# Kernel optimization log

Measured on AMD Instinct MI355X. Metric: run time of the kernel, lower is better.

Reference implementation:

```python
import jax, jax.numpy as jnp
import numpy as np

D = 1024
N_HEAD = 16
D_HEAD = D // N_HEAD


def setup_inputs() -> dict:
    key = jax.random.key(0)
    k1, k2, k3 = jax.random.split(key, 3)
    x = jax.random.normal(k1, (4, 2048, D), dtype=jnp.float32)
    # torch nn.Linear weights: [out_features, in_features]
    W_qkv = jax.random.normal(k2, (3 * D, D), dtype=jnp.float32) * (1.0 / np.sqrt(D))
    W_o = jax.random.normal(k3, (D, D), dtype=jnp.float32) * (1.0 / np.sqrt(D))
    return {"x": x, "W_qkv": W_qkv, "W_o": W_o}


def reference(x, W_qkv, W_o):
    b, s, d = x.shape
    qkv = x @ W_qkv.T                      # [b, s, 3d]
    q, k, v = jnp.split(qkv, 3, axis=-1)
    # [b, s, d] -> [b, h, s, dh]
    def heads(z):
        return z.reshape(b, s, N_HEAD, D_HEAD).transpose(0, 2, 1, 3)
    q, k, v = heads(q), heads(k), heads(v)
    scores = jnp.einsum("bhqd,bhkd->bhqk", q, k) / np.sqrt(D_HEAD).astype(np.float32)
    causal = jnp.tril(jnp.ones((s, s), dtype=bool))  # True = keep
    scores = jnp.where(causal, scores, -jnp.inf)
    attn = jax.nn.softmax(scores, axis=-1)
    out = jnp.einsum("bhqk,bhkd->bhqd", attn, v)     # [b, h, s, dh]
    out = out.transpose(0, 2, 1, 3).reshape(b, s, d)
    return out @ W_o.T
```

## Files before the change

### kernel.cpp

```cpp
#include <hip/hip_runtime.h>


typedef _Float16 f16x8 __attribute__((ext_vector_type(8)));
typedef float floatx4 __attribute__((ext_vector_type(4)));
typedef unsigned int uint2v __attribute__((ext_vector_type(2)));

union U4H8 { uint4 u; f16x8 h; };

__device__ __forceinline__ ushort f32_to_h_bits(float f) {
  _Float16 h = (_Float16)f;
  return __builtin_bit_cast(ushort, h);
}
__device__ __forceinline__ uint pack2h(float a, float b) {
  return (uint)f32_to_h_bits(a) | ((uint)f32_to_h_bits(b) << 16);
}
__device__ __forceinline__ float exp2_fast(float x) {
  float r;
  asm("v_exp_f32 %0, %1" : "=v"(r) : "v"(x));
  return r;
}

__device__ __forceinline__ void gld16(const void* g, void* l) {
  __builtin_amdgcn_global_load_lds(
      (const __attribute__((address_space(1))) unsigned char*)g,
      (__attribute__((address_space(3))) unsigned char*)l, 16, 0, 0);
}

__global__ __launch_bounds__(256) void cast_f32_f16(const float* __restrict__ in,
                                                    ushort* __restrict__ out) {
  int i = blockIdx.x * 256 + threadIdx.x;
  float4 v = ((const float4*)in)[i];
  ushort4 o;
  o.x = f32_to_h_bits(v.x);
  o.y = f32_to_h_bits(v.y);
  o.z = f32_to_h_bits(v.z);
  o.w = f32_to_h_bits(v.w);
  ((ushort4*)out)[i] = o;
}

template <int OUT_F16>
__global__ __launch_bounds__(256) void gemm_bt(const ushort* __restrict__ A,
                                               const ushort* __restrict__ B,
                                               void* __restrict__ Cv,
                                               int M, int N, int K) {
  __shared__ ushort As[128 * 32];
  __shared__ ushort Bs[128 * 32];

  const int tid = threadIdx.x;
  const int lane = tid & 63;
  const int wid = tid >> 6;
  const int l15 = lane & 15;
  const int quad = lane >> 4;
  const int m0 = blockIdx.y * 128;
  const int n0 = blockIdx.x * 128;
  const int wm = (wid & 1) * 64;
  const int wn = (wid >> 1) * 64;

  floatx4 acc[4][4];
#pragma unroll
  for (int i = 0; i < 4; i++)
#pragma unroll
    for (int j = 0; j < 4; j++) acc[i][j] = (floatx4){0.f, 0.f, 0.f, 0.f};

  const int srow = tid >> 2;
  const int scol = (tid & 3) * 8;
  const ushort* Ap0 = A + (size_t)(m0 + srow) * K + scol;
  const ushort* Ap1 = A + (size_t)(m0 + 64 + srow) * K + scol;
  const ushort* Bp0 = B + (size_t)(n0 + srow) * K + scol;
  const ushort* Bp1 = B + (size_t)(n0 + 64 + srow) * K + scol;
  ushort* AsW = As + wid * 512;
  ushort* BsW = Bs + wid * 512;

  for (int k0 = 0; k0 < K; k0 += 32) {
    __syncthreads();
    gld16(Ap0 + k0, AsW);
    gld16(Ap1 + k0, AsW + 2048);
    gld16(Bp0 + k0, BsW);
    gld16(Bp1 + k0, BsW + 2048);
    __syncthreads();

    U4H8 af[4], bf[4];
#pragma unroll
    for (int mi = 0; mi < 4; mi++)
      af[mi].u = *(const uint4*)&As[(wm + mi * 16 + l15) * 32 + quad * 8];
#pragma unroll
    for (int ni = 0; ni < 4; ni++)
      bf[ni].u = *(const uint4*)&Bs[(wn + ni * 16 + l15) * 32 + quad * 8];
#pragma unroll
    for (int mi = 0; mi < 4; mi++)
#pragma unroll
      for (int ni = 0; ni < 4; ni++)
        acc[mi][ni] = __builtin_amdgcn_mfma_f32_16x16x32_f16(af[mi].h, bf[ni].h,
                                                             acc[mi][ni], 0, 0, 0);
  }

#pragma unroll
  for (int mi = 0; mi < 4; mi++) {
#pragma unroll
    for (int r = 0; r < 4; r++) {
      size_t row = m0 + wm + mi * 16 + quad * 4 + r;
#pragma unroll
      for (int ni = 0; ni < 4; ni++) {
        size_t col = n0 + wn + ni * 16 + l15;
        float v = acc[mi][ni][r];
        if (OUT_F16)
          ((ushort*)Cv)[row * N + col] = f32_to_h_bits(v);
        else
          ((float*)Cv)[row * N + col] = v;
      }
    }
  }
}

__global__ __launch_bounds__(256) void vtrans(const ushort* __restrict__ qkv,
                                              ushort* __restrict__ vtg) {
  __shared__ ushort T[64 * 66];
  const int tid = threadIdx.x;
  const int kt = blockIdx.x;
  const int bh = blockIdx.y;
  const int b = bh >> 4, h = bh & 15;

  const int r = tid >> 3;
  const int c = (tid & 7) * 8;
  const ushort* src = qkv + (size_t)(b * 2048 + kt * 64) * 3072 + 2048 + h * 64;
  uint4 v0 = *(const uint4*)(src + (size_t)r * 3072 + c);
  uint4 v1 = *(const uint4*)(src + (size_t)(r + 32) * 3072 + c);
  union { uint4 u; ushort s[8]; } a0, a1;
  a0.u = v0; a1.u = v1;
#pragma unroll
  for (int j = 0; j < 8; j++) {
    T[(c + j) * 66 + r] = a0.s[j];
    T[(c + j) * 66 + r + 32] = a1.s[j];
  }
  __syncthreads();

  const int d = tid >> 3;
  const int kc = (tid & 7) * 8;
  ushort* dst = vtg + (size_t)bh * 64 * 2048 + (size_t)kt * 64;
  union { uint u[4]; uint4 u4; } o0, o1;
#pragma unroll
  for (int i = 0; i < 4; i++) {
    o0.u[i] = *(const uint*)&T[d * 66 + kc + 2 * i];
    o1.u[i] = *(const uint*)&T[(d + 32) * 66 + kc + 2 * i];
  }
  *(uint4*)(dst + (size_t)d * 2048 + kc) = o0.u4;
  *(uint4*)(dst + (size_t)(d + 32) * 2048 + kc) = o1.u4;
}

__global__ __launch_bounds__(256, 4) void attn_fused(const ushort* __restrict__ qkv,
                                                     const ushort* __restrict__ vtg,
                                                     ushort* __restrict__ attn_out) {
  __shared__ ushort Ks[2][4096];
  __shared__ ushort Vs[2][4096];
  __shared__ ushort Ps[4][16 * 40];

  const int tid = threadIdx.x;
  const int lane = tid & 63;
  const int w = tid >> 6;
  const int l15 = lane & 15;
  const int quad = lane >> 4;
  const int id = blockIdx.x;
  const int n_ = id >> 3;
  const int bx = n_ >> 3;
  const int bh = (id & 7) * 8 + (n_ & 7);
  const int b = bh >> 4;
  const int h = bh & 15;
  const int bS = b * 2048;
  const int qtA = bx;
  const int qtB = 31 - bx;
  const int ktmax = qtB;
  int q0s[2];
  q0s[0] = qtA * 64 + w * 16;
  q0s[1] = qtB * 64 + w * 16;

  U4H8 qf[2][2];
#pragma unroll
  for (int s = 0; s < 2; s++) {
    const ushort* qrow = qkv + (size_t)(bS + q0s[s] + l15) * 3072 + h * 64;
#pragma unroll
    for (int kc = 0; kc < 2; kc++) {
      qf[s][kc].u = *(const uint4*)(qrow + kc * 32 + quad * 8);
      qf[s][kc].h = qf[s][kc].h * (_Float16)0.1803368787f;
    }
  }

  floatx4 o[2][4];
#pragma unroll
  for (int s = 0; s < 2; s++)
#pragma unroll
    for (int ni = 0; ni < 4; ni++) o[s][ni] = (floatx4){0.f, 0.f, 0.f, 0.f};
  float m_i[2] = {-1e30f, -1e30f}, l_i[2] = {0.f, 0.f};

  const ushort* kbase = qkv + (size_t)bS * 3072 + 1024 + h * 64;
  const ushort* vbase = vtg + (size_t)bh * 64 * 2048;
  const int sr = lane & 15;
  const int scc = (lane >> 4) * 8;

  auto stage = [&](int kt, int buf) {
    const ushort* kg = kbase + (size_t)(kt * 64 + w * 16 + sr) * 3072 + scc;
    gld16(kg, &Ks[buf][(w * 2 + 0) * 512]);
    gld16(kg + 32, &Ks[buf][(w * 2 + 1) * 512]);
    const ushort* vg = vbase + (size_t)(w * 16 + sr) * 2048 + (size_t)kt * 64 + scc;
    gld16(vg, &Vs[buf][(w * 2 + 0) * 512]);
    gld16(vg + 32, &Vs[buf][(w * 2 + 1) * 512]);
  };

  auto strip_step = [&](int s, bool diag, int kt64, int buf) {
    floatx4 s4[4];
    __builtin_amdgcn_s_setprio(1);
#pragma unroll
    for (int t = 0; t < 4; t++) {
      U4H8 kf0, kf1;
      kf0.u = *(const uint4*)&Ks[buf][(t * 2 + 0) * 512 + lane * 8];
      kf1.u = *(const uint4*)&Ks[buf][(t * 2 + 1) * 512 + lane * 8];
      floatx4 sa = (floatx4){0.f, 0.f, 0.f, 0.f};
      sa = __builtin_amdgcn_mfma_f32_16x16x32_f16(kf0.h, qf[s][0].h, sa, 0, 0, 0);
      sa = __builtin_amdgcn_mfma_f32_16x16x32_f16(kf1.h, qf[s][1].h, sa, 0, 0, 0);
      s4[t] = sa;
    }
    __builtin_amdgcn_s_setprio(0);
    if (diag) {
      const int q = q0s[s] + l15;
#pragma unroll
      for (int t = 0; t < 4; t++)
#pragma unroll
        for (int r = 0; r < 4; r++) {
          int key = kt64 + t * 16 + quad * 4 + r;
          if (key > q) s4[t][r] = -1e30f;
        }
    }

    float tmax = -1e30f;
#pragma unroll
    for (int t = 0; t < 4; t++)
#pragma unroll
      for (int r = 0; r < 4; r++) tmax = fmaxf(tmax, s4[t][r]);
    tmax = fmaxf(tmax, __shfl_xor(tmax, 16));
    tmax = fmaxf(tmax, __shfl_xor(tmax, 32));
    if (__any(tmax > m_i[s])) {
      float mnew = fmaxf(m_i[s], tmax);
      float alpha = exp2_fast(m_i[s] - mnew);
      m_i[s] = mnew;
      l_i[s] *= alpha;
#pragma unroll
      for (int ni = 0; ni < 4; ni++) o[s][ni] *= alpha;
    }
    const float m2 = m_i[s];
    float rs = 0.f;
#pragma unroll
    for (int t = 0; t < 4; t++)
#pragma unroll
      for (int r = 0; r < 4; r++) {
        float p = exp2_fast(s4[t][r] - m2);
        s4[t][r] = p;
        rs += p;
      }
    rs += __shfl_xor(rs, 16);
    rs += __shfl_xor(rs, 32);
    l_i[s] += rs;

#pragma unroll
    for (int kc = 0; kc < 2; kc++) {
      uint pA = pack2h(s4[kc * 2][0], s4[kc * 2][1]);
      uint pB = pack2h(s4[kc * 2][2], s4[kc * 2][3]);
      uint pC = pack2h(s4[kc * 2 + 1][0], s4[kc * 2 + 1][1]);
      uint pD = pack2h(s4[kc * 2 + 1][2], s4[kc * 2 + 1][3]);
      uint2v ac = __builtin_amdgcn_permlane32_swap(pA, pC, false, false);
      uint2v bd = __builtin_amdgcn_permlane32_swap(pB, pD, false, false);
      uint2v ac2 = __builtin_amdgcn_permlane16_swap(ac[0], ac[1], false, false);
      uint2v bd2 = __builtin_amdgcn_permlane16_swap(bd[0], bd[1], false, false);
      U4H8 pb;
      pb.u = (uint4){ac2[0], bd2[0], ac2[1], bd2[1]};
      __builtin_amdgcn_s_setprio(1);
#pragma unroll
      for (int ni = 0; ni < 4; ni++) {
        U4H8 vf;
        vf.u = *(const uint4*)&Vs[buf][(ni * 2 + kc) * 512 + lane * 8];
        o[s][ni] = __builtin_amdgcn_mfma_f32_16x16x32_f16(vf.h, pb.h, o[s][ni], 0, 0, 0);
      }
      __builtin_amdgcn_s_setprio(0);
    }
  };

  stage(0, 0);
  for (int kt = 0; kt <= ktmax; ++kt) {
    const int buf = kt & 1;
    __syncthreads();
    if (kt < ktmax) stage(kt + 1, buf ^ 1);
    strip_step(1, kt == qtB, kt * 64, buf);
    if (kt <= qtA) strip_step(0, kt == qtA, kt * 64, buf);
  }

#pragma unroll
  for (int s = 0; s < 2; s++) {
    float inv = 1.0f / l_i[s];
    ushort* orow = attn_out + (size_t)(bS + q0s[s] + l15) * 1024 + h * 64;
#pragma unroll
    for (int p = 0; p < 2; p++) {
#pragma unroll
      for (int nh = 0; nh < 2; nh++) {
        const int ni = p * 2 + nh;
        *(uint*)&Ps[w][l15 * 40 + nh * 16 + quad * 4] =
            pack2h(o[s][ni][0] * inv, o[s][ni][1] * inv);
        *(uint*)&Ps[w][l15 * 40 + nh * 16 + quad * 4 + 2] =
            pack2h(o[s][ni][2] * inv, o[s][ni][3] * inv);
      }
      __asm__ volatile("s_waitcnt lgkmcnt(0)" ::: "memory");
      uint4 x = *(const uint4*)&Ps[w][l15 * 40 + quad * 8];
      *(uint4*)(orow + p * 32 + quad * 8) = x;
      __asm__ volatile("s_waitcnt lgkmcnt(0)" ::: "memory");
    }
  }
}

extern "C" void kernel_launch(void* const* d_in, const int* in_sizes, int n_in,
                              void* d_out, int out_size, void* d_ws, size_t ws_size,
                              hipStream_t stream) {
  const float* x = (const float*)d_in[0];
  const float* wqkv = (const float*)d_in[1];
  const float* wo = (const float*)d_in[2];
  float* out = (float*)d_out;

  ushort* xh = (ushort*)d_ws;
  ushort* wqkvh = xh + (size_t)8192 * 1024;
  ushort* woh = wqkvh + (size_t)3072 * 1024;
  ushort* qkvh = woh + (size_t)1024 * 1024;
  ushort* attnh = qkvh + (size_t)8192 * 3072;
  ushort* vtg = attnh + (size_t)8192 * 1024;

  cast_f32_f16<<<8192, 256, 0, stream>>>(x, xh);
  cast_f32_f16<<<3072, 256, 0, stream>>>(wqkv, wqkvh);
  cast_f32_f16<<<1024, 256, 0, stream>>>(wo, woh);

  gemm_bt<1><<<dim3(24, 64), 256, 0, stream>>>(xh, wqkvh, qkvh, 8192, 3072, 1024);
  vtrans<<<dim3(32, 64), 256, 0, stream>>>(qkvh, vtg);
  attn_fused<<<dim3(1024), 256, 0, stream>>>(qkvh, vtg, attnh);
  gemm_bt<0><<<dim3(8, 64), 256, 0, stream>>>(attnh, woh, out, 8192, 1024, 1024);
}
```

Measured before the change: 270.2 us.

## Double-buffer GEMM LDS tiles, remap block order, use conflict-free fragment layout

The GEMM kernel now keeps two LDS buffers and issues the global-to-LDS loads for the next K slice before computing the current one, with one barrier per iteration instead of two. Block indices are remapped so that consecutive blocks are spread across eight groups, aiming for better L2 locality across XCDs. The LDS layout changes so each wave stores a 16-row fragment contiguously, letting each lane read its 16-byte fragment at lane*8 without bank conflicts. The costs are double the LDS per block, which may reduce occupancy, and a grid remap that assumes the block count divides by eight.

```diff
diff --git a/kernel.cpp b/kernel.cpp
--- a/kernel.cpp
+++ b/kernel.cpp
@@ -43,18 +43,24 @@
                                                const ushort* __restrict__ B,
                                                void* __restrict__ Cv,
                                                int M, int N, int K) {
-  __shared__ ushort As[128 * 32];
-  __shared__ ushort Bs[128 * 32];
+  __shared__ ushort As[2][4096];
+  __shared__ ushort Bs[2][4096];
 
   const int tid = threadIdx.x;
   const int lane = tid & 63;
-  const int wid = tid >> 6;
+  const int w = tid >> 6;
   const int l15 = lane & 15;
   const int quad = lane >> 4;
-  const int m0 = blockIdx.y * 128;
-  const int n0 = blockIdx.x * 128;
-  const int wm = (wid & 1) * 64;
-  const int wn = (wid >> 1) * 64;
+
+  const int gx = gridDim.x;
+  const int lin = blockIdx.y * gx + blockIdx.x;
+  const int qq = (gx * gridDim.y) >> 3;
+  const int nl = (lin & 7) * qq + (lin >> 3);
+  const int m0 = (nl / gx) * 128;
+  const int n0 = (nl % gx) * 128;
+
+  const int wm = (w & 1) * 64;
+  const int wn = (w >> 1) * 64;
 
   floatx4 acc[4][4];
 #pragma unroll
@@ -62,30 +68,37 @@
 #pragma unroll
     for (int j = 0; j < 4; j++) acc[i][j] = (floatx4){0.f, 0.f, 0.f, 0.f};
 
-  const int srow = tid >> 2;
-  const int scol = (tid & 3) * 8;
-  const ushort* Ap0 = A + (size_t)(m0 + srow) * K + scol;
-  const ushort* Ap1 = A + (size_t)(m0 + 64 + srow) * K + scol;
-  const ushort* Bp0 = B + (size_t)(n0 + srow) * K + scol;
-  const ushort* Bp1 = B + (size_t)(n0 + 64 + srow) * K + scol;
-  ushort* AsW = As + wid * 512;
-  ushort* BsW = Bs + wid * 512;
-
-  for (int k0 = 0; k0 < K; k0 += 32) {
-    __syncthreads();
-    gld16(Ap0 + k0, AsW);
-    gld16(Ap1 + k0, AsW + 2048);
-    gld16(Bp0 + k0, BsW);
-    gld16(Bp1 + k0, BsW + 2048);
-    __syncthreads();
+  const int sr = lane & 15;
+  const int sc = (lane >> 4) * 8;
+  const ushort* Ap = A + (size_t)(m0 + w * 16 + sr) * K + sc;
+  const ushort* Bp = B + (size_t)(n0 + w * 16 + sr) * K + sc;
+  const size_t rstep = (size_t)64 * K;
+
+  auto stage = [&](int k0, int buf) {
+    gld16(Ap + k0, &As[buf][w * 512]);
+    gld16(Ap + rstep + k0, &As[buf][(w + 4) * 512]);
+    gld16(Bp + k0, &Bs[buf][w * 512]);
+    gld16(Bp + rstep + k0, &Bs[buf][(w + 4) * 512]);
+  };
+
+  stage(0, 0);
+  const int hA = (w & 1) * 4;
+  const int hB = (w >> 1) * 4;
+
+  for (int k0 = 0, t = 0; k0 < K; k0 += 32, ++t) {
+    const int buf = t & 1;
+    asm volatile("s_waitcnt vmcnt(0)" ::: "memory");
+    __builtin_amdgcn_s_barrier();
+    asm volatile("" ::: "memory");
+    if (k0 + 32 < K) stage(k0 + 32, buf ^ 1);
 
     U4H8 af[4], bf[4];
 #pragma unroll
     for (int mi = 0; mi < 4; mi++)
-      af[mi].u = *(const uint4*)&As[(wm + mi * 16 + l15) * 32 + quad * 8];
+      af[mi].u = *(const uint4*)&As[buf][(hA + mi) * 512 + lane * 8];
 #pragma unroll
     for (int ni = 0; ni < 4; ni++)
-      bf[ni].u = *(const uint4*)&Bs[(wn + ni * 16 + l15) * 32 + quad * 8];
+      bf[ni].u = *(const uint4*)&Bs[buf][(hB + ni) * 512 + lane * 8];
 #pragma unroll
     for (int mi = 0; mi < 4; mi++)
 #pragma unroll
```

Result: slower. 298.0 us (+10.3%).
